# Kernel optimization log

Measured on AMD Instinct MI355X. Metric: run time of the kernel, lower is better.

Reference implementation:

```python
import jax, jax.numpy as jnp
import numpy as np

B, N, M, D = 16, 4096, 4096, 3

def setup_inputs() -> dict:
    key = jax.random.key(0)
    k1, k2 = jax.random.split(key)
    x = jax.random.normal(k1, (B, N, D), dtype=jnp.float32)
    y = jax.random.normal(k2, (B, M, D), dtype=jnp.float32)
    return {"x": x, "y": y}

def reference(x, y):
    # pairwise L2 distance matrix C: [B, N, M]
    diff = x[:, :, None, :] - y[:, None, :, :]          # [B, N, M, D]
    C = jnp.sqrt(jnp.sum(diff * diff, axis=-1))          # [B, N, M]
    d1 = jnp.min(C, axis=-1).mean(axis=-1)               # x -> nearest y, mean over N: [B]
    d2 = jnp.min(C, axis=-2).mean(axis=-1)               # y -> nearest x, mean over M: [B]
    cost = (d1 + d2) / 2.0                               # reduction='none'
    return cost
```

## Files before the change

### kernel.cpp

```cpp
#include <hip/hip_runtime.h>
#include <cstdint>
#include <cstddef>

#define S      4096
#define BATCH  16
#define BLK    256
#define YSPAN  1024
#define NT_TOT (YSPAN / 32)
#define ROWS_PER_BLOCK 128
#define XC_N   (S / ROWS_PER_BLOCK)
#define YC_N   (S / YSPAN)

typedef _Float16 half8   __attribute__((ext_vector_type(8)));
typedef float    floatx16 __attribute__((ext_vector_type(16)));

__device__ inline unsigned pack2(_Float16 lo, _Float16 hi) {
    unsigned short a = __builtin_bit_cast(unsigned short, lo);
    unsigned short b = __builtin_bit_cast(unsigned short, hi);
    return (unsigned)a | ((unsigned)b << 16);
}

__global__ __launch_bounds__(BLK, 4) void chamfer_mfma_kernel(
    const float* __restrict__ x, const float* __restrict__ y,
    float* __restrict__ ws0, float* __restrict__ ws1,
    float* __restrict__ out)
{
    const int b    = blockIdx.y;
    const int xc   = blockIdx.x;
    const int role = blockIdx.z >> 2;
    const int slab = blockIdx.z & 3;
    const int tid  = threadIdx.x;
    const int lane = tid & 63;
    const int wave = tid >> 6;
    const int hi32 = lane >> 5;
    const int l31  = lane & 31;

    const float* __restrict__ outer = role ? y : x;
    const float* __restrict__ inner = role ? x : y;
    float* __restrict__ ws = role ? ws1 : ws0;

    if (xc == 0 && blockIdx.z == 0 && tid == 0) out[b] = 0.0f;

    __shared__ uint4 ldsb[NT_TOT][64];

    for (int i = tid; i < NT_TOT * 32; i += BLK) {
        ldsb[i >> 5][32 + (i & 31)].z = 0x00003C00u;
        ldsb[i >> 5][32 + (i & 31)].w = 0u;
    }

    const int row = xc * ROWS_PER_BLOCK + wave * 32 + l31;
    const float* op = outer + ((size_t)b * S + row) * 3;
    const float o0 = op[0], o1 = op[1], o2 = op[2];
    const float on = 0.5f * (o0 * o0 + o1 * o1 + o2 * o2);
    const _Float16 oh0 = (_Float16)o0, oh1 = (_Float16)o1, oh2 = (_Float16)o2;
    const _Float16 ol0 = (_Float16)(o0 - (float)oh0);
    const _Float16 ol1 = (_Float16)(o1 - (float)oh1);
    const _Float16 ol2 = (_Float16)(o2 - (float)oh2);
    const _Float16 onh = (_Float16)on;
    const _Float16 onl = (_Float16)(on - (float)onh);
    half8 afrag;
    if (hi32 == 0) {
        afrag[0] = -oh0; afrag[1] = -oh1; afrag[2] = -oh2;
        afrag[3] = -oh0; afrag[4] = -oh1; afrag[5] = -oh2;
        afrag[6] = -ol0; afrag[7] = -ol1;
    } else {
        afrag[0] = -ol2; afrag[1] = (_Float16)1.0f; afrag[2] = (_Float16)1.0f;
        afrag[3] = onh;  afrag[4] = onl;
        afrag[5] = (_Float16)0.0f; afrag[6] = (_Float16)0.0f; afrag[7] = (_Float16)0.0f;
    }

    const float* isrc = inner + ((size_t)b * S + slab * YSPAN) * 3;
#pragma unroll
    for (int k = 0; k < YSPAN / BLK; ++k) {
        const int p = k * BLK + tid;
        const float* ip = isrc + (size_t)p * 3;
        const float i0 = ip[0], i1 = ip[1], i2 = ip[2];
        const float h  = 0.5f * (i0 * i0 + i1 * i1 + i2 * i2);
        const _Float16 a0 = (_Float16)i0, a1 = (_Float16)i1, a2 = (_Float16)i2;
        const _Float16 b0 = (_Float16)(i0 - (float)a0);
        const _Float16 b1 = (_Float16)(i1 - (float)a1);
        const _Float16 b2 = (_Float16)(i2 - (float)a2);
        const _Float16 hh = (_Float16)h;
        const _Float16 hl = (_Float16)(h - (float)hh);
        const int t = p >> 5, col = p & 31;
        ldsb[t][col] = make_uint4(pack2(a0, a1), pack2(a2, b0),
                                  pack2(b1, b2), pack2(a0, a1));
        *(uint2*)&ldsb[t][32 + col] =
            make_uint2(pack2(a2, hh), pack2(hl, (_Float16)1.0f));
    }

    __syncthreads();

    floatx16 runrow;
#pragma unroll
    for (int r = 0; r < 16; ++r) runrow[r] = 3.0e38f;
    const floatx16 zeroacc = {};

#pragma unroll 4
    for (int t = 0; t < NT_TOT; ++t) {
        const uint4 braw = ldsb[t][lane];
        const half8 bfrag = __builtin_bit_cast(half8, braw);
        const floatx16 d =
            __builtin_amdgcn_mfma_f32_32x32x16_f16(afrag, bfrag, zeroacc, 0, 0, 0);
#pragma unroll
        for (int r = 0; r < 16; ++r) runrow[r] = fminf(runrow[r], d[r]);
    }

#pragma unroll
    for (int r = 0; r < 16; ++r) {
        float v = runrow[r];
        v = fminf(v, __shfl_xor(v, 1));
        v = fminf(v, __shfl_xor(v, 2));
        v = fminf(v, __shfl_xor(v, 4));
        v = fminf(v, __shfl_xor(v, 8));
        v = fminf(v, __shfl_xor(v, 16));
        runrow[r] = v;
    }
    if (l31 == 0) {
        float* w = ws + ((size_t)slab * BATCH + b) * S
                      + xc * ROWS_PER_BLOCK + wave * 32;
#pragma unroll
        for (int r = 0; r < 16; ++r) {
            const int rr = (r & 3) + 8 * (r >> 2) + 4 * hi32;
            w[rr] = runrow[r];
        }
    }
}

#define RSEG   (S / BLK)
__global__ __launch_bounds__(BLK) void chamfer_reduce_kernel(
    const float* __restrict__ ws0, const float* __restrict__ ws1,
    float* __restrict__ out)
{
    const int b   = blockIdx.y;
    const int i   = blockIdx.x * BLK + threadIdx.x;
    const int tid = threadIdx.x;

    float mx = 3.0e38f, my = 3.0e38f;
#pragma unroll
    for (int sl = 0; sl < YC_N; ++sl) {
        mx = fminf(mx, ws0[((size_t)sl * BATCH + b) * S + i]);
        my = fminf(my, ws1[((size_t)sl * BATCH + b) * S + i]);
    }

    float s = sqrtf(2.0f * fmaxf(mx, 0.0f)) + sqrtf(2.0f * fmaxf(my, 0.0f));

    __shared__ float red[BLK];
    red[tid] = s;
    __syncthreads();
    for (int off = BLK / 2; off > 0; off >>= 1) {
        if (tid < off) red[tid] += red[tid + off];
        __syncthreads();
    }
    if (tid == 0) atomicAdd(&out[b], red[0] * (0.5f / (float)S));
}

#define P   8
#define FMC 1024
#define OUTER_PER_BLK (BLK * P)
__global__ __launch_bounds__(BLK) void chamfer_full_kernel(
    const float* __restrict__ x, const float* __restrict__ y,
    float* __restrict__ out)
{
    const int role = blockIdx.z;
    const int b    = blockIdx.y;
    const int oc   = blockIdx.x;
    const float* __restrict__ outer = (role == 0) ? x : y;
    const float* __restrict__ inner = (role == 0) ? y : x;
    const int tid = threadIdx.x;
    const int n0  = oc * OUTER_PER_BLK;

    __shared__ float4 lds[FMC];

    float nx0[P], nx1[P], nx2[P], xn[P], tmin[P];
#pragma unroll
    for (int p = 0; p < P; ++p) {
        const int n = n0 + p * BLK + tid;
        const float* xp = outer + ((size_t)b * S + n) * 3;
        const float a0 = xp[0], a1 = xp[1], a2 = xp[2];
        nx0[p] = -a0; nx1[p] = -a1; nx2[p] = -a2;
        xn[p]  = a0 * a0 + a1 * a1 + a2 * a2;
        tmin[p] = 3.0e38f;
    }

    for (int m0 = 0; m0 < S; m0 += FMC) {
        __syncthreads();
        for (int i = tid; i < FMC; i += BLK) {
            const float* yp = inner + ((size_t)b * S + m0 + i) * 3;
            const float a0 = yp[0], a1 = yp[1], a2 = yp[2];
            lds[i] = make_float4(a0, a1, a2,
                                 0.5f * (a0 * a0 + a1 * a1 + a2 * a2));
        }
        __syncthreads();
#pragma unroll 4
        for (int j = 0; j < FMC; ++j) {
            const float4 v = lds[j];
#pragma unroll
            for (int p = 0; p < P; ++p) {
                const float t = fmaf(nx0[p], v.x,
                                 fmaf(nx1[p], v.y,
                                  fmaf(nx2[p], v.z, v.w)));
                tmin[p] = fminf(tmin[p], t);
            }
        }
    }

    float s = 0.0f;
#pragma unroll
    for (int p = 0; p < P; ++p)
        s += sqrtf(fmaxf(fmaf(2.0f, tmin[p], xn[p]), 0.0f));

    __shared__ float red[BLK];
    red[tid] = s;
    __syncthreads();
    for (int off = BLK / 2; off > 0; off >>= 1) {
        if (tid < off) red[tid] += red[tid + off];
        __syncthreads();
    }
    if (tid == 0) atomicAdd(&out[b], red[0] * (0.5f / (float)S));
}

extern "C" void kernel_launch(void* const* d_in, const int* in_sizes, int n_in,
                              void* d_out, int out_size, void* d_ws, size_t ws_size,
                              hipStream_t stream) {
    const float* x = (const float*)d_in[0];
    const float* y = (const float*)d_in[1];
    float* out = (float*)d_out;

    const size_t n_ws = (size_t)YC_N * BATCH * S;
    const size_t need = 2 * n_ws * sizeof(float);
    if (ws_size >= need) {
        float* ws0 = (float*)d_ws;
        float* ws1 = ws0 + n_ws;
        chamfer_mfma_kernel<<<dim3(XC_N, BATCH, 2 * YC_N), BLK, 0, stream>>>(
            x, y, ws0, ws1, out);
        chamfer_reduce_kernel<<<dim3(RSEG, BATCH), BLK, 0, stream>>>(
            ws0, ws1, out);
    } else {
        hipMemsetAsync(d_out, 0, BATCH * sizeof(float), stream);
        chamfer_full_kernel<<<dim3(S / OUTER_PER_BLK, BATCH, 2), BLK, 0, stream>>>(
            x, y, out);
    }
}
```

Before: 39.66 us.

## Halve y-span per block and software-pipeline MFMA with min folding

Cuts the inner span per block from 1024 to 512 points, which doubles the number of slabs and the grid size. The MFMA loop is restructured into two in-flight accumulators, so each MFMA is issued while the previous result is folded into the running minimum, hiding MFMA latency. The launch-bounds occupancy hint rises from 4 to 5. The smaller span means more partial-min writes and a heavier reduce stage (it still reads only YC_N slabs, which stays consistent because YC_N follows YSPAN), and register pressure rises.

Result: slower. 47.53 us (+19.8%).

```diff
diff --git a/kernel.cpp b/kernel.cpp
--- a/kernel.cpp
+++ b/kernel.cpp
@@ -5,7 +5,7 @@
 #define S      4096
 #define BATCH  16
 #define BLK    256
-#define YSPAN  1024
+#define YSPAN  512
 #define NT_TOT (YSPAN / 32)
 #define ROWS_PER_BLOCK 128
 #define XC_N   (S / ROWS_PER_BLOCK)
@@ -20,15 +20,21 @@
     return (unsigned)a | ((unsigned)b << 16);
 }
 
-__global__ __launch_bounds__(BLK, 4) void chamfer_mfma_kernel(
+#define FOLD(dd)                                                        \
+    {                                                                   \
+        _Pragma("unroll")                                               \
+        for (int r = 0; r < 16; ++r) runrow[r] = fminf(runrow[r], dd[r]); \
+    }
+
+__global__ __launch_bounds__(BLK, 5) void chamfer_mfma_kernel(
     const float* __restrict__ x, const float* __restrict__ y,
     float* __restrict__ ws0, float* __restrict__ ws1,
     float* __restrict__ out)
 {
     const int b    = blockIdx.y;
     const int xc   = blockIdx.x;
-    const int role = blockIdx.z >> 2;
-    const int slab = blockIdx.z & 3;
+    const int role = blockIdx.z >> 3;
+    const int slab = blockIdx.z & 7;
     const int tid  = threadIdx.x;
     const int lane = tid & 63;
     const int wave = tid >> 6;
@@ -94,16 +100,27 @@
     floatx16 runrow;
 #pragma unroll
     for (int r = 0; r < 16; ++r) runrow[r] = 3.0e38f;
-    const floatx16 zeroacc = {};
-
-#pragma unroll 4
-    for (int t = 0; t < NT_TOT; ++t) {
-        const uint4 braw = ldsb[t][lane];
-        const half8 bfrag = __builtin_bit_cast(half8, braw);
-        const floatx16 d =
-            __builtin_amdgcn_mfma_f32_32x32x16_f16(afrag, bfrag, zeroacc, 0, 0, 0);
-#pragma unroll
-        for (int r = 0; r < 16; ++r) runrow[r] = fminf(runrow[r], d[r]);
+    const floatx16 z16 = {};
+
+    uint4 b0 = ldsb[0][lane];
+    floatx16 d0 =
+        __builtin_amdgcn_mfma_f32_32x32x16_f16(afrag, __builtin_bit_cast(half8, b0), z16, 0, 0, 0);
+    uint4 b1 = ldsb[1][lane];
+    floatx16 d1 =
+        __builtin_amdgcn_mfma_f32_32x32x16_f16(afrag, __builtin_bit_cast(half8, b1), z16, 0, 0, 0);
+
+#pragma unroll
+    for (int t = 0; t < NT_TOT; t += 2) {
+        if (t + 2 < NT_TOT) b0 = ldsb[t + 2][lane];
+        FOLD(d0);
+        if (t + 2 < NT_TOT)
+            d0 = __builtin_amdgcn_mfma_f32_32x32x16_f16(
+                afrag, __builtin_bit_cast(half8, b0), z16, 0, 0, 0);
+        if (t + 3 < NT_TOT) b1 = ldsb[t + 3][lane];
+        FOLD(d1);
+        if (t + 3 < NT_TOT)
+            d1 = __builtin_amdgcn_mfma_f32_32x32x16_f16(
+                afrag, __builtin_bit_cast(half8, b1), z16, 0, 0, 0);
     }
 
 #pragma unroll
```

## Switch pairwise-distance MFMA from 32x32x16 to 16x16x32 with repacked fragments

Applied to the files above, without the earlier changes.

Replaces the 32x32x16 f16 MFMA tile with the 16x16x32 variant. The 32-wide K dimension holds the hi/lo split coordinates and norm terms, with each wave now owning 16 outer rows. The LDS layout for inner points is repacked to match, and two MFMAs are issued per loop step before their results are min-reduced. Rows per block drop to 64 and the occupancy hint rises from 4 to 5, which doubles the grid and shrinks the per-lane min/shuffle work. The cost is twice as many blocks, so each block's inner-point staging is repeated more often.

After: 46.03 us. 1.16x slower.

```diff
diff --git a/kernel.cpp b/kernel.cpp
--- a/kernel.cpp
+++ b/kernel.cpp
@@ -6,13 +6,13 @@
 #define BATCH  16
 #define BLK    256
 #define YSPAN  1024
-#define NT_TOT (YSPAN / 32)
-#define ROWS_PER_BLOCK 128
+#define NT16   (YSPAN / 16)
+#define ROWS_PER_BLOCK 64
 #define XC_N   (S / ROWS_PER_BLOCK)
 #define YC_N   (S / YSPAN)
 
 typedef _Float16 half8   __attribute__((ext_vector_type(8)));
-typedef float    floatx16 __attribute__((ext_vector_type(16)));
+typedef float    floatx4 __attribute__((ext_vector_type(4)));
 
 __device__ inline unsigned pack2(_Float16 lo, _Float16 hi) {
     unsigned short a = __builtin_bit_cast(unsigned short, lo);
@@ -20,7 +20,7 @@
     return (unsigned)a | ((unsigned)b << 16);
 }
 
-__global__ __launch_bounds__(BLK, 4) void chamfer_mfma_kernel(
+__global__ __launch_bounds__(BLK, 5) void chamfer_mfma_kernel(
     const float* __restrict__ x, const float* __restrict__ y,
     float* __restrict__ ws0, float* __restrict__ ws1,
     float* __restrict__ out)
@@ -32,7 +32,8 @@
     const int tid  = threadIdx.x;
     const int lane = tid & 63;
     const int wave = tid >> 6;
-    const int hi32 = lane >> 5;
+    const int l15  = lane & 15;
+    const int g    = lane >> 4;
     const int l31  = lane & 31;
 
     const float* __restrict__ outer = role ? y : x;
@@ -41,14 +42,9 @@
 
     if (xc == 0 && blockIdx.z == 0 && tid == 0) out[b] = 0.0f;
 
-    __shared__ uint4 ldsb[NT_TOT][64];
-
-    for (int i = tid; i < NT_TOT * 32; i += BLK) {
-        ldsb[i >> 5][32 + (i & 31)].z = 0x00003C00u;
-        ldsb[i >> 5][32 + (i & 31)].w = 0u;
-    }
-
-    const int row = xc * ROWS_PER_BLOCK + wave * 32 + l31;
+    __shared__ uint4 ldsb[NT16 * 32];
+
+    const int row = xc * ROWS_PER_BLOCK + wave * 16 + l15;
     const float* op = outer + ((size_t)b * S + row) * 3;
     const float o0 = op[0], o1 = op[1], o2 = op[2];
     const float on = 0.5f * (o0 * o0 + o1 * o1 + o2 * o2);
@@ -58,15 +54,20 @@
     const _Float16 ol2 = (_Float16)(o2 - (float)oh2);
     const _Float16 onh = (_Float16)on;
     const _Float16 onl = (_Float16)(on - (float)onh);
+    const _Float16 h1c = (_Float16)1.0f;
+    const _Float16 h0c = (_Float16)0.0f;
     half8 afrag;
-    if (hi32 == 0) {
+    if (g == 0) {
         afrag[0] = -oh0; afrag[1] = -oh1; afrag[2] = -oh2;
-        afrag[3] = -oh0; afrag[4] = -oh1; afrag[5] = -oh2;
-        afrag[6] = -ol0; afrag[7] = -ol1;
+        afrag[3] = -ol0; afrag[4] = -ol1; afrag[5] = -ol2;
+        afrag[6] = onh;  afrag[7] = onl;
+    } else if (g == 1) {
+        afrag[0] = -oh0; afrag[1] = -oh1; afrag[2] = -oh2;
+        afrag[3] = h1c;  afrag[4] = h1c;
+        afrag[5] = h0c;  afrag[6] = h0c;  afrag[7] = h0c;
     } else {
-        afrag[0] = -ol2; afrag[1] = (_Float16)1.0f; afrag[2] = (_Float16)1.0f;
-        afrag[3] = onh;  afrag[4] = onl;
-        afrag[5] = (_Float16)0.0f; afrag[6] = (_Float16)0.0f; afrag[7] = (_Float16)0.0f;
+        afrag[0] = h0c; afrag[1] = h0c; afrag[2] = h0c; afrag[3] = h0c;
+        afrag[4] = h0c; afrag[5] = h0c; afrag[6] = h0c; afrag[7] = h0c;
     }
 
     const float* isrc = inner + ((size_t)b * S + slab * YSPAN) * 3;
@@ -77,53 +78,52 @@
         const float i0 = ip[0], i1 = ip[1], i2 = ip[2];
         const float h  = 0.5f * (i0 * i0 + i1 * i1 + i2 * i2);
         const _Float16 a0 = (_Float16)i0, a1 = (_Float16)i1, a2 = (_Float16)i2;
-        const _Float16 b0 = (_Float16)(i0 - (float)a0);
-        const _Float16 b1 = (_Float16)(i1 - (float)a1);
-        const _Float16 b2 = (_Float16)(i2 - (float)a2);
+        const _Float16 c0 = (_Float16)(i0 - (float)a0);
+        const _Float16 c1 = (_Float16)(i1 - (float)a1);
+        const _Float16 c2 = (_Float16)(i2 - (float)a2);
         const _Float16 hh = (_Float16)h;
         const _Float16 hl = (_Float16)(h - (float)hh);
-        const int t = p >> 5, col = p & 31;
-        ldsb[t][col] = make_uint4(pack2(a0, a1), pack2(a2, b0),
-                                  pack2(b1, b2), pack2(a0, a1));
-        *(uint2*)&ldsb[t][32 + col] =
-            make_uint2(pack2(a2, hh), pack2(hl, (_Float16)1.0f));
+        const int t = p >> 4, col = p & 15;
+        ldsb[t * 32 + col]      = make_uint4(pack2(a0, a1), pack2(a2, a0),
+                                             pack2(a1, a2), pack2(h1c, h1c));
+        ldsb[t * 32 + 16 + col] = make_uint4(pack2(c0, c1), pack2(c2, hh),
+                                             pack2(hl, h0c), pack2(h0c, h0c));
     }
 
     __syncthreads();
 
-    floatx16 runrow;
-#pragma unroll
-    for (int r = 0; r < 16; ++r) runrow[r] = 3.0e38f;
-    const floatx16 zeroacc = {};
-
-#pragma unroll 4
-    for (int t = 0; t < NT_TOT; ++t) {
-        const uint4 braw = ldsb[t][lane];
-        const half8 bfrag = __builtin_bit_cast(half8, braw);
-        const floatx16 d =
-            __builtin_amdgcn_mfma_f32_32x32x16_f16(afrag, bfrag, zeroacc, 0, 0, 0);
-#pragma unroll
-        for (int r = 0; r < 16; ++r) runrow[r] = fminf(runrow[r], d[r]);
-    }
-
-#pragma unroll
-    for (int r = 0; r < 16; ++r) {
-        float v = runrow[r];
+    floatx4 run;
+#pragma unroll
+    for (int r = 0; r < 4; ++r) run[r] = 3.0e38f;
+    const floatx4 z4 = {};
+
+#pragma unroll 2
+    for (int t = 0; t < NT16; t += 2) {
+        const uint4 q0 = ldsb[t * 32 + l31];
+        const uint4 q1 = ldsb[(t + 1) * 32 + l31];
+        const floatx4 d0 = __builtin_amdgcn_mfma_f32_16x16x32_f16(
+            afrag, __builtin_bit_cast(half8, q0), z4, 0, 0, 0);
+        const floatx4 d1 = __builtin_amdgcn_mfma_f32_16x16x32_f16(
+            afrag, __builtin_bit_cast(half8, q1), z4, 0, 0, 0);
+#pragma unroll
+        for (int r = 0; r < 4; ++r)
+            run[r] = fminf(fminf(d0[r], d1[r]), run[r]);
+    }
+
+#pragma unroll
+    for (int r = 0; r < 4; ++r) {
+        float v = run[r];
         v = fminf(v, __shfl_xor(v, 1));
         v = fminf(v, __shfl_xor(v, 2));
         v = fminf(v, __shfl_xor(v, 4));
         v = fminf(v, __shfl_xor(v, 8));
-        v = fminf(v, __shfl_xor(v, 16));
-        runrow[r] = v;
-    }
-    if (l31 == 0) {
+        run[r] = v;
+    }
+    if (l15 == 0) {
         float* w = ws + ((size_t)slab * BATCH + b) * S
-                      + xc * ROWS_PER_BLOCK + wave * 32;
-#pragma unroll
-        for (int r = 0; r < 16; ++r) {
-            const int rr = (r & 3) + 8 * (r >> 2) + 4 * hi32;
-            w[rr] = runrow[r];
-        }
+                      + xc * ROWS_PER_BLOCK + wave * 16 + g * 4;
+#pragma unroll
+        for (int r = 0; r < 4; ++r) w[r] = run[r];
     }
 }
 
```
